# Kernel tuning notes

Hardware: AMD Instinct MI355X
Metric: run time of the kernel (lower is better)

Reference implementation:

```python
import jax, jax.numpy as jnp
import numpy as np

DIM = 1024
HEADS = 16
HEAD_DIM = DIM // HEADS
THRESH = 0.29514
SHARP = 15.0
LN_EPS = 1e-5
NORM_EPS = 1e-12


def setup_inputs() -> dict:
    key = jax.random.key(0)
    ks = jax.random.split(key, 8)
    s = 1.0 / np.sqrt(DIM)
    sg = 1.0 / np.sqrt(HEAD_DIM)
    return {
        "x": jax.random.normal(ks[0], (2, 2048, DIM), dtype=jnp.float32),
        "Wq": jax.random.uniform(ks[1], (DIM, DIM), jnp.float32, -s, s),
        "Wk": jax.random.uniform(ks[2], (DIM, DIM), jnp.float32, -s, s),
        "Wv": jax.random.uniform(ks[3], (DIM, DIM), jnp.float32, -s, s),
        "gq": jax.random.uniform(ks[4], (HEAD_DIM,), jnp.float32, -sg, sg),
        "gk": jax.random.uniform(ks[5], (HEAD_DIM,), jnp.float32, -sg, sg),
        "Wo": jax.random.uniform(ks[6], (DIM, DIM), jnp.float32, -s, s),
        "bo": jax.random.uniform(ks[7], (DIM,), jnp.float32, -s, s),
        "ln_w": jnp.ones((DIM,), jnp.float32),
        "ln_b": jnp.zeros((DIM,), jnp.float32),
    }


def _l2norm(t):
    # F.normalize: t / max(||t||_2, eps)
    n = jnp.sqrt(jnp.sum(t * t, axis=-1, keepdims=True))
    return t / jnp.maximum(n, NORM_EPS)


def reference(x, Wq, Wk, Wv, gq, gk, Wo, bo, ln_w, ln_b):
    B, T, D = x.shape
    # LayerNorm over last dim
    mu = jnp.mean(x, axis=-1, keepdims=True)
    var = jnp.mean((x - mu) ** 2, axis=-1, keepdims=True)
    x_norm = (x - mu) / jnp.sqrt(var + LN_EPS) * ln_w + ln_b

    def split_heads(t):  # [B,T,D] -> [B,H,T,hd]
        return t.reshape(B, T, HEADS, HEAD_DIM).transpose(0, 2, 1, 3)

    q = _l2norm(split_heads(x_norm @ Wq))
    k = _l2norm(split_heads(x_norm @ Wk))
    v = split_heads(x @ Wv)  # note: v uses un-normalized x, as in source

    align = jnp.einsum("bhtd,bhsd->bhts", q, k)  # cosine alignment
    resonance = jax.nn.sigmoid((align - THRESH) * SHARP)
    gate_q = jnp.einsum("bhtd,d->bht", q, gq)
    gate_k = jnp.einsum("bhsd,d->bhs", k, gk)
    modulation = resonance * gate_q[..., :, None] * gate_k[..., None, :]
    collapse = jnp.einsum("bhts,bhsd->bhtd", modulation, v)
    collapse = collapse.transpose(0, 2, 1, 3).reshape(B, T, D)
    return collapse @ Wo + bo
```

## Files before the change

### kernel.cpp

```cpp
#include <hip/hip_runtime.h>
#include <math.h>

#define DIM 1024
#define T_SEQ 2048
#define NBATCH 2
#define HEADS 16
#define HD 64
#define NTOK 4096
#define THRESH 0.29514f
#define SHARP 15.0f
#define LOG2E 1.4426950408889634f

typedef __attribute__((ext_vector_type(8))) short bf16x8;
typedef __attribute__((ext_vector_type(4))) float f32x4;
typedef __attribute__((ext_vector_type(4))) unsigned int u32x4;

__device__ __forceinline__ unsigned short f2b(float f) {
    unsigned int u = __float_as_uint(f);
    unsigned int r = (u + 0x7FFFu + ((u >> 16) & 1u)) >> 16;
    return (unsigned short)r;
}
__device__ __forceinline__ float b2f(unsigned short u) {
    return __uint_as_float(((unsigned int)u) << 16);
}
__device__ __forceinline__ unsigned int pack2_bf16(float lo, float hi) {
    unsigned int a = __float_as_uint(lo) + 0x8000u;
    unsigned int b = __float_as_uint(hi) + 0x8000u;
    return __builtin_amdgcn_perm(b, a, 0x07060302u);
}

__device__ __forceinline__ void async_cp16(const unsigned short* g, unsigned short* l) {
    __builtin_amdgcn_global_load_lds(
        (const __attribute__((address_space(1))) unsigned int*)g,
        (__attribute__((address_space(3))) unsigned int*)l, 16, 0, 0);
}

__global__ __launch_bounds__(256) void ln_xnorm_kernel(
    const float* __restrict__ x, const float* __restrict__ lnw, const float* __restrict__ lnb,
    unsigned short* __restrict__ xnb, unsigned short* __restrict__ xb) {
    int row = blockIdx.x * 4 + (threadIdx.x >> 6);
    int lane = threadIdx.x & 63;
    const float4* xr = (const float4*)(x + (size_t)row * DIM);
    float4 v[4];
    float s = 0.f, ss = 0.f;
#pragma unroll
    for (int i = 0; i < 4; i++) {
        v[i] = xr[lane + i * 64];
        s += v[i].x + v[i].y + v[i].z + v[i].w;
        ss += v[i].x * v[i].x + v[i].y * v[i].y + v[i].z * v[i].z + v[i].w * v[i].w;
    }
#pragma unroll
    for (int off = 32; off; off >>= 1) {
        s += __shfl_xor(s, off);
        ss += __shfl_xor(ss, off);
    }
    float m = s * (1.f / DIM);
    float rstd = rsqrtf(ss * (1.f / DIM) - m * m + 1e-5f);
#pragma unroll
    for (int i = 0; i < 4; i++) {
        int e = (lane + i * 64) * 4;
        float4 lw = *(const float4*)&lnw[e];
        float4 lb = *(const float4*)&lnb[e];
        ushort4 un, ur;
        un.x = f2b((v[i].x - m) * rstd * lw.x + lb.x);
        un.y = f2b((v[i].y - m) * rstd * lw.y + lb.y);
        un.z = f2b((v[i].z - m) * rstd * lw.z + lb.z);
        un.w = f2b((v[i].w - m) * rstd * lw.w + lb.w);
        ur.x = f2b(v[i].x); ur.y = f2b(v[i].y); ur.z = f2b(v[i].z); ur.w = f2b(v[i].w);
        *(ushort4*)&xnb[(size_t)row * DIM + e] = un;
        *(ushort4*)&xb[(size_t)row * DIM + e] = ur;
    }
}

__global__ __launch_bounds__(256) void wtrans_kernel(
    const float* __restrict__ W0, const float* __restrict__ W1,
    const float* __restrict__ W2, const float* __restrict__ W3,
    unsigned short* __restrict__ T0, unsigned short* __restrict__ T1,
    unsigned short* __restrict__ T2, unsigned short* __restrict__ T3) {
    __shared__ float tile[64][65];
    const int z = blockIdx.z;
    const float* W = (z == 0) ? W0 : (z == 1) ? W1 : (z == 2) ? W2 : W3;
    unsigned short* T = (z == 0) ? T0 : (z == 1) ? T1 : (z == 2) ? T2 : T3;
    const int k0 = blockIdx.x * 64, n0 = blockIdx.y * 64;
    const int r = threadIdx.x >> 3;
    const int c = (threadIdx.x & 7) * 8;
#pragma unroll
    for (int half = 0; half < 2; half++) {
        int rr = r + half * 32;
        float4 a = *(const float4*)&W[(size_t)(k0 + rr) * DIM + n0 + c];
        float4 b = *(const float4*)&W[(size_t)(k0 + rr) * DIM + n0 + c + 4];
        tile[rr][c + 0] = a.x; tile[rr][c + 1] = a.y; tile[rr][c + 2] = a.z; tile[rr][c + 3] = a.w;
        tile[rr][c + 4] = b.x; tile[rr][c + 5] = b.y; tile[rr][c + 6] = b.z; tile[rr][c + 7] = b.w;
    }
    __syncthreads();
#pragma unroll
    for (int half = 0; half < 2; half++) {
        int dd = r + half * 32;
        bf16x8 o;
#pragma unroll
        for (int j = 0; j < 8; j++) o[j] = (short)f2b(tile[c + j][dd]);
        *(bf16x8*)&T[(size_t)(n0 + dd) * DIM + k0 + c] = o;
    }
}

template <int MODE>
__global__ __launch_bounds__(256) void gemm_mfma_kernel(
    const unsigned short* __restrict__ A0, const unsigned short* __restrict__ A2,
    const unsigned short* __restrict__ Bt0, const unsigned short* __restrict__ Bt1,
    const unsigned short* __restrict__ Bt2, const float* __restrict__ bias,
    const float* __restrict__ gq, const float* __restrict__ gk,
    unsigned short* __restrict__ Oq, unsigned short* __restrict__ Ok,
    unsigned short* __restrict__ Ov, float* __restrict__ gq_t, float* __restrict__ gk_t,
    float* __restrict__ Oout) {
    constexpr int NT = (MODE == 0) ? 4 : 2;
    __shared__ __align__(16) unsigned short As[2][128 * 32];
    __shared__ __align__(16) unsigned short Bs[2][NT * 32 * 32];
    const int tid = threadIdx.x;
    const int lane = tid & 63, w = tid >> 6;
    const int l16 = lane & 15, quad = lane >> 4;
    const int wm = w >> 1, wn = w & 1;
    int m0, n0, z = 0;
    if constexpr (MODE == 0) {
        const int f = blockIdx.x + (blockIdx.y << 5) + (blockIdx.z << 8);
        const int ww = (f & 7) * 96 + (f >> 3);
        z = ww >> 8;
        m0 = ((ww >> 3) & 31) * 128;
        n0 = (ww & 7) * 128;
    } else {
        const int f = blockIdx.x + (blockIdx.y << 5);
        const int ww = (f & 7) * 64 + (f >> 3);
        m0 = (ww >> 4) * 128;
        n0 = (ww & 15) * 64;
    }
    const unsigned short* A;
    const unsigned short* Bt;
    if constexpr (MODE == 0) {
        A = (z == 2) ? A2 : A0;
        Bt = (z == 0) ? Bt0 : (z == 1) ? Bt1 : Bt2;
    } else {
        A = A0;
        Bt = Bt0;
    }
    f32x4 acc[4][NT] = {};
    const int kswz = (l16 >> 1) & 3;

    const int lin0 = tid, lin1 = 256 + tid;
    const int sm0 = lin0 >> 2, sk0 = (lin0 & 3) ^ ((sm0 >> 1) & 3);
    const int sm1 = lin1 >> 2, sk1 = (lin1 & 3) ^ ((sm1 >> 1) & 3);

    auto stage = [&](int kb, int k0) {
        async_cp16(A + (size_t)(m0 + sm0) * DIM + k0 + sk0 * 8, &As[kb][lin0 * 8]);
        async_cp16(A + (size_t)(m0 + sm1) * DIM + k0 + sk1 * 8, &As[kb][lin1 * 8]);
        async_cp16(Bt + (size_t)(n0 + sm0) * DIM + k0 + sk0 * 8, &Bs[kb][lin0 * 8]);
        if constexpr (MODE == 0)
            async_cp16(Bt + (size_t)(n0 + sm1) * DIM + k0 + sk1 * 8, &Bs[kb][lin1 * 8]);
    };

    stage(0, 0);
    __syncthreads();

    for (int ks = 0; ks < DIM / 32; ks++) {
        const int cur = ks & 1;
        if (ks + 1 < DIM / 32) stage(cur ^ 1, (ks + 1) * 32);
        bf16x8 af[4], bfr[NT];
#pragma unroll
        for (int t = 0; t < 4; t++) {
            int ma = wm * 64 + t * 16 + l16;
            af[t] = *(const bf16x8*)(&As[cur][ma * 32 + ((quad ^ kswz) * 8)]);
        }
#pragma unroll
        for (int t = 0; t < NT; t++) {
            int nb = wn * (NT * 16) + t * 16 + l16;
            bfr[t] = *(const bf16x8*)(&Bs[cur][nb * 32 + ((quad ^ kswz) * 8)]);
        }
#pragma unroll
        for (int mt = 0; mt < 4; mt++)
#pragma unroll
            for (int nt = 0; nt < NT; nt++)
                acc[mt][nt] =
                    __builtin_amdgcn_mfma_f32_16x16x32_bf16(af[mt], bfr[nt], acc[mt][nt], 0, 0, 0);
        __syncthreads();
    }

    if constexpr (MODE == 0) {
        const int h = (n0 + wn * 64) >> 6;
        if (z <= 1) {
            constexpr float QSCALE = -SHARP * LOG2E;
            const float* gvec = (z == 0) ? gq : gk;
            float* gate = (z == 0) ? gq_t : gk_t;
            unsigned short* O = (z == 0) ? Oq : Ok;
            const float oscale = (z == 0) ? QSCALE : 1.0f;
            float gv[4];
#pragma unroll
            for (int nt = 0; nt < 4; nt++) gv[nt] = gvec[nt * 16 + l16];
#pragma unroll
            for (int mt = 0; mt < 4; mt++) {
#pragma unroll
                for (int r = 0; r < 4; r++) {
                    float ss = 0.f;
#pragma unroll
                    for (int nt = 0; nt < 4; nt++) ss += acc[mt][nt][r] * acc[mt][nt][r];
#pragma unroll
                    for (int msk = 1; msk < 16; msk <<= 1) ss += __shfl_xor(ss, msk);
                    float rn = __builtin_amdgcn_rcpf(fmaxf(sqrtf(ss), 1e-12f));
                    float vn[4], gg = 0.f;
#pragma unroll
                    for (int nt = 0; nt < 4; nt++) {
                        vn[nt] = acc[mt][nt][r] * rn;
                        gg += vn[nt] * gv[nt];
                    }
#pragma unroll
                    for (int msk = 1; msk < 16; msk <<= 1) gg += __shfl_xor(gg, msk);
                    int tok = m0 + wm * 64 + mt * 16 + quad * 4 + r;
                    int b = tok >> 11, t = tok & 2047;
                    size_t rowbase = ((size_t)(b * HEADS + h) * T_SEQ + t) * HD;
#pragma unroll
                    for (int nt = 0; nt < 4; nt++)
                        O[rowbase + nt * 16 + l16] = f2b(vn[nt] * oscale);
                    if (l16 == 0) gate[(b * HEADS + h) * T_SEQ + t] = gg;
                }
            }
        } else {
#pragma unroll
            for (int mt = 0; mt < 4; mt++) {
#pragma unroll
                for (int r = 0; r < 4; r++) {
                    int tok = m0 + wm * 64 + mt * 16 + quad * 4 + r;
                    int b = tok >> 11, t = tok & 2047;
                    size_t rowbase = ((size_t)(b * HEADS + h) * T_SEQ + t) * HD;
#pragma unroll
                    for (int nt = 0; nt < 4; nt++)
                        Ov[rowbase + nt * 16 + l16] = f2b(acc[mt][nt][r]);
                }
            }
        }
    } else {
        float bias_r[NT];
#pragma unroll
        for (int nt = 0; nt < NT; nt++) bias_r[nt] = bias[n0 + wn * (NT * 16) + nt * 16 + l16];
#pragma unroll
        for (int mt = 0; mt < 4; mt++) {
#pragma unroll
            for (int r = 0; r < 4; r++) {
                int tok = m0 + wm * 64 + mt * 16 + quad * 4 + r;
#pragma unroll
                for (int nt = 0; nt < NT; nt++) {
                    int n = n0 + wn * (NT * 16) + nt * 16 + l16;
                    Oout[(size_t)tok * DIM + n] = acc[mt][nt][r] + bias_r[nt];
                }
            }
        }
    }
}

__global__ __launch_bounds__(256) void vtrans_kernel(const unsigned short* __restrict__ Vn,
                                                     const float* __restrict__ gk_t,
                                                     unsigned short* __restrict__ Vt) {
    __shared__ float tile[64][65];
    const int bh = blockIdx.y;
    const int t0 = blockIdx.x * 64;
    const int r = threadIdx.x >> 3;
    const int c = (threadIdx.x & 7) * 8;
    const unsigned short* src = Vn + (size_t)bh * T_SEQ * HD;
#pragma unroll
    for (int half = 0; half < 2; half++) {
        int rr = r + half * 32;
        float gkv = gk_t[bh * T_SEQ + t0 + rr];
        bf16x8 v = *(const bf16x8*)(src + (size_t)(t0 + rr) * HD + c);
#pragma unroll
        for (int j = 0; j < 8; j++) tile[rr][c + j] = b2f((unsigned short)v[j]) * gkv;
    }
    __syncthreads();
    unsigned short* dst = Vt + (size_t)bh * HD * T_SEQ;
#pragma unroll
    for (int half = 0; half < 2; half++) {
        int dd = r + half * 32;
        bf16x8 o;
#pragma unroll
        for (int j = 0; j < 8; j++) o[j] = (short)f2b(tile[c + j][dd]);
        *(bf16x8*)(dst + (size_t)dd * T_SEQ + t0 + c) = o;
    }
}

__global__ __launch_bounds__(256, 4) void attn_mfma_kernel(
    const unsigned short* __restrict__ Qn, const unsigned short* __restrict__ Kn,
    const unsigned short* __restrict__ Vt, const float* __restrict__ gateq,
    unsigned short* __restrict__ collp0, unsigned short* __restrict__ collp1) {
    __shared__ __align__(16) unsigned short Ks[2][64 * 64];
    __shared__ __align__(16) unsigned short VtL[2][64 * 64];
    const int tid = threadIdx.x;
    const int lane = tid & 63, w = tid >> 6;
    const int quad = lane >> 4, l16 = lane & 15;
    const int f = blockIdx.x + 16 * blockIdx.y + 256 * blockIdx.z;
    const int q_ = f >> 3;
    const int panel = (f & 7) * 8 + (q_ >> 4);
    const int t0 = (q_ & 15) * 128;
    const int h = panel & 15;
    const int zz = panel >> 4;
    const int b = zz >> 1, shalf = zz & 1;
    const int sbase = shalf * (T_SEQ / 2);
    const int bh = b * HEADS + h;
    const size_t base = (size_t)bh * T_SEQ * HD;
    constexpr float K0 = THRESH * SHARP * LOG2E;
    const f32x4 k0v = {K0, K0, K0, K0};

    int det0 = quad, det1 = quad + 4;
    asm("v_permlane16_swap_b32 %0, %1" : "+v"(det0), "+v"(det1));
    const bool flagA = (__builtin_amdgcn_readfirstlane(det0) == 0);

    bf16x8 fq[2][2];
#pragma unroll
    for (int mt = 0; mt < 2; mt++) {
        const unsigned short* qrow = Qn + base + (size_t)(t0 + w * 32 + mt * 16 + l16) * HD;
        fq[mt][0] = *(const bf16x8*)(qrow + quad * 8);
        fq[mt][1] = *(const bf16x8*)(qrow + 32 + quad * 8);
    }

    f32x4 oacc[4][2] = {};
    const int srow = tid >> 3;
    const int sgp = tid & 7;
    const int swz = l16 & 7;

    auto stage_chunk = [&](unsigned short* ksn, unsigned short* vtn, int s0) {
#pragma unroll
        for (int half = 0; half < 2; half++) {
            int row = srow + half * 32;
            int g = sgp ^ (row & 7);
            async_cp16(Kn + base + (size_t)(s0 + row) * HD + g * 8, ksn + row * 64 + sgp * 8);
            async_cp16(Vt + base + (size_t)row * T_SEQ + s0 + g * 8, vtn + row * 64 + sgp * 8);
        }
    };

    auto do_chunk = [&](const unsigned short* ksb, const unsigned short* vtb) {
#pragma unroll
        for (int kh = 0; kh < 2; kh++) {
            unsigned int p[2][2][2];
#pragma unroll
            for (int ct2 = 0; ct2 < 2; ct2++) {
                const int ct = 2 * kh + ct2;
                const unsigned short* krow = ksb + (ct * 16 + l16) * 64;
                bf16x8 fk0 = *(const bf16x8*)(krow + (quad ^ swz) * 8);
                bf16x8 fk1 = *(const bf16x8*)(krow + ((quad + 4) ^ swz) * 8);
#pragma unroll
                for (int mt = 0; mt < 2; mt++) {
                    __builtin_amdgcn_s_setprio(1);
                    f32x4 s1 =
                        __builtin_amdgcn_mfma_f32_16x16x32_bf16(fk0, fq[mt][0], k0v, 0, 0, 0);
                    f32x4 sacc =
                        __builtin_amdgcn_mfma_f32_16x16x32_bf16(fk1, fq[mt][1], s1, 0, 0, 0);
                    __builtin_amdgcn_s_setprio(0);
                    float w0 = __builtin_amdgcn_rcpf(1.f + __builtin_amdgcn_exp2f(sacc[0]));
                    float w1 = __builtin_amdgcn_rcpf(1.f + __builtin_amdgcn_exp2f(sacc[1]));
                    float w2 = __builtin_amdgcn_rcpf(1.f + __builtin_amdgcn_exp2f(sacc[2]));
                    float w3 = __builtin_amdgcn_rcpf(1.f + __builtin_amdgcn_exp2f(sacc[3]));
                    p[mt][ct2][0] = pack2_bf16(w0, w1);
                    p[mt][ct2][1] = pack2_bf16(w2, w3);
                }
            }
            int gv = (4 * kh + 2 * (quad & 1) + (quad >> 1)) ^ swz;
            bf16x8 fv[4];
#pragma unroll
            for (int dt = 0; dt < 4; dt++)
                fv[dt] = *(const bf16x8*)(vtb + (dt * 16 + l16) * 64 + gv * 8);
#pragma unroll
            for (int mt = 0; mt < 2; mt++) {
                unsigned int aL = p[mt][0][0], aH = p[mt][0][1];
                unsigned int bL = p[mt][1][0], bH = p[mt][1][1];
                asm("v_permlane16_swap_b32 %0, %1" : "+v"(aL), "+v"(bL));
                asm("v_permlane16_swap_b32 %0, %1" : "+v"(aH), "+v"(bH));
                u32x4 bt;
                if (flagA) {
                    bt.x = aL; bt.y = aH; bt.z = bL; bt.w = bH;
                } else {
                    bt.x = bL; bt.y = bH; bt.z = aL; bt.w = aH;
                }
                bf16x8 fs = __builtin_bit_cast(bf16x8, bt);
                __builtin_amdgcn_s_setprio(1);
#pragma unroll
                for (int dt = 0; dt < 4; dt++)
                    oacc[dt][mt] =
                        __builtin_amdgcn_mfma_f32_16x16x32_bf16(fv[dt], fs, oacc[dt][mt], 0, 0, 0);
                __builtin_amdgcn_s_setprio(0);
            }
        }
        __syncthreads();
    };

    stage_chunk(&Ks[0][0], &VtL[0][0], sbase);
    __syncthreads();

    for (int j = 0; j < T_SEQ / 256; j++) {
        stage_chunk(&Ks[1][0], &VtL[1][0], sbase + j * 128 + 64);
        do_chunk(&Ks[0][0], &VtL[0][0]);
        if (j + 1 < T_SEQ / 256) stage_chunk(&Ks[0][0], &VtL[0][0], sbase + j * 128 + 128);
        do_chunk(&Ks[1][0], &VtL[1][0]);
    }

    unsigned short* collp = shalf ? collp1 : collp0;
#pragma unroll
    for (int mt = 0; mt < 2; mt++) {
        int t = t0 + w * 32 + mt * 16 + l16;
        float gq_v = gateq[bh * T_SEQ + t];
        unsigned short* dst = collp + ((size_t)b * T_SEQ + t) * DIM + h * HD;
#pragma unroll
        for (int dt = 0; dt < 4; dt++) {
            ushort4 o;
            o.x = f2b(oacc[dt][mt][0] * gq_v);
            o.y = f2b(oacc[dt][mt][1] * gq_v);
            o.z = f2b(oacc[dt][mt][2] * gq_v);
            o.w = f2b(oacc[dt][mt][3] * gq_v);
            *(ushort4*)(dst + dt * 16 + quad * 4) = o;
        }
    }
}

__global__ __launch_bounds__(256) void merge_kernel(unsigned short* __restrict__ p0,
                                                    const unsigned short* __restrict__ p1) {
    size_t i = ((size_t)blockIdx.x * 256 + threadIdx.x) * 8;
    bf16x8 a = *(const bf16x8*)(p0 + i);
    bf16x8 c = *(const bf16x8*)(p1 + i);
    bf16x8 o;
#pragma unroll
    for (int j = 0; j < 8; j++)
        o[j] = (short)f2b(b2f((unsigned short)a[j]) + b2f((unsigned short)c[j]));
    *(bf16x8*)(p0 + i) = o;
}

extern "C" void kernel_launch(void* const* d_in, const int* in_sizes, int n_in,
                              void* d_out, int out_size, void* d_ws, size_t ws_size,
                              hipStream_t stream) {
    const float* x = (const float*)d_in[0];
    const float* Wq = (const float*)d_in[1];
    const float* Wk = (const float*)d_in[2];
    const float* Wv = (const float*)d_in[3];
    const float* gq = (const float*)d_in[4];
    const float* gk = (const float*)d_in[5];
    const float* Wo = (const float*)d_in[6];
    const float* bo = (const float*)d_in[7];
    const float* lnw = (const float*)d_in[8];
    const float* lnb = (const float*)d_in[9];
    float* out = (float*)d_out;

    unsigned short* ws = (unsigned short*)d_ws;
    unsigned short* xnb = ws;
    unsigned short* xb = xnb + (size_t)NTOK * DIM;
    unsigned short* Wqt = xb + (size_t)NTOK * DIM;
    unsigned short* Wkt = Wqt + (size_t)DIM * DIM;
    unsigned short* Wvt = Wkt + (size_t)DIM * DIM;
    unsigned short* Wot = Wvt + (size_t)DIM * DIM;
    unsigned short* Q16 = Wot + (size_t)DIM * DIM;
    unsigned short* K16 = Q16 + (size_t)NTOK * DIM;
    unsigned short* Vn = K16 + (size_t)NTOK * DIM;
    float* gq_t = (float*)(Vn + (size_t)NTOK * DIM);
    float* gk_t = gq_t + NBATCH * HEADS * T_SEQ;
    unsigned short* collb1 = (unsigned short*)(gk_t + NBATCH * HEADS * T_SEQ);
    unsigned short* Vt = xnb;
    unsigned short* collb0 = xb;

    ln_xnorm_kernel<<<NTOK / 4, 256, 0, stream>>>(x, lnw, lnb, xnb, xb);
    wtrans_kernel<<<dim3(16, 16, 4), 256, 0, stream>>>(Wq, Wk, Wv, Wo, Wqt, Wkt, Wvt, Wot);
    gemm_mfma_kernel<0><<<dim3(NTOK / 128, DIM / 128, 3), 256, 0, stream>>>(
        xnb, xb, Wqt, Wkt, Wvt, nullptr, gq, gk, Q16, K16, Vn, gq_t, gk_t, nullptr);
    vtrans_kernel<<<dim3(T_SEQ / 64, NBATCH * HEADS), 256, 0, stream>>>(Vn, gk_t, Vt);
    attn_mfma_kernel<<<dim3(T_SEQ / 128, HEADS, NBATCH * 2), 256, 0, stream>>>(
        Q16, K16, Vt, gq_t, collb0, collb1);
    merge_kernel<<<(NTOK * DIM) / (256 * 8), 256, 0, stream>>>(collb0, collb1);
    gemm_mfma_kernel<1><<<dim3(NTOK / 128, DIM / 64, 1), 256, 0, stream>>>(
        collb0, nullptr, Wot, nullptr, nullptr, bo, nullptr, nullptr, nullptr, nullptr, nullptr,
        nullptr, nullptr, out);
}
```

Before: 222.0 us.

## Fuse LN and weight-transpose launches; fold split-K merge into output GEMM A-load

Merges the LayerNorm and weight-transpose kernels into a single launch that branches on block index. It also removes the separate merge kernel by having the output-projection GEMM read both partial attention outputs through registers, sum them, and write the result to LDS. This replaces its async copy for A. The aim is to save two launches and one full read-write pass over the collapse buffer. The cost is that the output GEMM's A loads become synchronous register loads with extra conversion ALU, and each row is re-summed once per N tile.

```diff
diff --git a/kernel.cpp b/kernel.cpp
--- a/kernel.cpp
+++ b/kernel.cpp
@@ -35,71 +35,72 @@
         (__attribute__((address_space(3))) unsigned int*)l, 16, 0, 0);
 }
 
-__global__ __launch_bounds__(256) void ln_xnorm_kernel(
+__global__ __launch_bounds__(256) void prep_kernel(
     const float* __restrict__ x, const float* __restrict__ lnw, const float* __restrict__ lnb,
-    unsigned short* __restrict__ xnb, unsigned short* __restrict__ xb) {
-    int row = blockIdx.x * 4 + (threadIdx.x >> 6);
-    int lane = threadIdx.x & 63;
-    const float4* xr = (const float4*)(x + (size_t)row * DIM);
-    float4 v[4];
-    float s = 0.f, ss = 0.f;
-#pragma unroll
-    for (int i = 0; i < 4; i++) {
-        v[i] = xr[lane + i * 64];
-        s += v[i].x + v[i].y + v[i].z + v[i].w;
-        ss += v[i].x * v[i].x + v[i].y * v[i].y + v[i].z * v[i].z + v[i].w * v[i].w;
-    }
-#pragma unroll
-    for (int off = 32; off; off >>= 1) {
-        s += __shfl_xor(s, off);
-        ss += __shfl_xor(ss, off);
-    }
-    float m = s * (1.f / DIM);
-    float rstd = rsqrtf(ss * (1.f / DIM) - m * m + 1e-5f);
-#pragma unroll
-    for (int i = 0; i < 4; i++) {
-        int e = (lane + i * 64) * 4;
-        float4 lw = *(const float4*)&lnw[e];
-        float4 lb = *(const float4*)&lnb[e];
-        ushort4 un, ur;
-        un.x = f2b((v[i].x - m) * rstd * lw.x + lb.x);
-        un.y = f2b((v[i].y - m) * rstd * lw.y + lb.y);
-        un.z = f2b((v[i].z - m) * rstd * lw.z + lb.z);
-        un.w = f2b((v[i].w - m) * rstd * lw.w + lb.w);
-        ur.x = f2b(v[i].x); ur.y = f2b(v[i].y); ur.z = f2b(v[i].z); ur.w = f2b(v[i].w);
-        *(ushort4*)&xnb[(size_t)row * DIM + e] = un;
-        *(ushort4*)&xb[(size_t)row * DIM + e] = ur;
-    }
-}
-
-__global__ __launch_bounds__(256) void wtrans_kernel(
+    unsigned short* __restrict__ xnb, unsigned short* __restrict__ xb,
     const float* __restrict__ W0, const float* __restrict__ W1,
     const float* __restrict__ W2, const float* __restrict__ W3,
     unsigned short* __restrict__ T0, unsigned short* __restrict__ T1,
     unsigned short* __restrict__ T2, unsigned short* __restrict__ T3) {
     __shared__ float tile[64][65];
-    const int z = blockIdx.z;
-    const float* W = (z == 0) ? W0 : (z == 1) ? W1 : (z == 2) ? W2 : W3;
-    unsigned short* T = (z == 0) ? T0 : (z == 1) ? T1 : (z == 2) ? T2 : T3;
-    const int k0 = blockIdx.x * 64, n0 = blockIdx.y * 64;
-    const int r = threadIdx.x >> 3;
-    const int c = (threadIdx.x & 7) * 8;
-#pragma unroll
-    for (int half = 0; half < 2; half++) {
-        int rr = r + half * 32;
-        float4 a = *(const float4*)&W[(size_t)(k0 + rr) * DIM + n0 + c];
-        float4 b = *(const float4*)&W[(size_t)(k0 + rr) * DIM + n0 + c + 4];
-        tile[rr][c + 0] = a.x; tile[rr][c + 1] = a.y; tile[rr][c + 2] = a.z; tile[rr][c + 3] = a.w;
-        tile[rr][c + 4] = b.x; tile[rr][c + 5] = b.y; tile[rr][c + 6] = b.z; tile[rr][c + 7] = b.w;
-    }
-    __syncthreads();
-#pragma unroll
-    for (int half = 0; half < 2; half++) {
-        int dd = r + half * 32;
-        bf16x8 o;
-#pragma unroll
-        for (int j = 0; j < 8; j++) o[j] = (short)f2b(tile[c + j][dd]);
-        *(bf16x8*)&T[(size_t)(n0 + dd) * DIM + k0 + c] = o;
+    if (blockIdx.x < 1024) {
+        int row = blockIdx.x * 4 + (threadIdx.x >> 6);
+        int lane = threadIdx.x & 63;
+        const float4* xr = (const float4*)(x + (size_t)row * DIM);
+        float4 v[4];
+        float s = 0.f, ss = 0.f;
+#pragma unroll
+        for (int i = 0; i < 4; i++) {
+            v[i] = xr[lane + i * 64];
+            s += v[i].x + v[i].y + v[i].z + v[i].w;
+            ss += v[i].x * v[i].x + v[i].y * v[i].y + v[i].z * v[i].z + v[i].w * v[i].w;
+        }
+#pragma unroll
+        for (int off = 32; off; off >>= 1) {
+            s += __shfl_xor(s, off);
+            ss += __shfl_xor(ss, off);
+        }
+        float m = s * (1.f / DIM);
+        float rstd = rsqrtf(ss * (1.f / DIM) - m * m + 1e-5f);
+#pragma unroll
+        for (int i = 0; i < 4; i++) {
+            int e = (lane + i * 64) * 4;
+            float4 lw = *(const float4*)&lnw[e];
+            float4 lb = *(const float4*)&lnb[e];
+            ushort4 un, ur;
+            un.x = f2b((v[i].x - m) * rstd * lw.x + lb.x);
+            un.y = f2b((v[i].y - m) * rstd * lw.y + lb.y);
+            un.z = f2b((v[i].z - m) * rstd * lw.z + lb.z);
+            un.w = f2b((v[i].w - m) * rstd * lw.w + lb.w);
+            ur.x = f2b(v[i].x); ur.y = f2b(v[i].y); ur.z = f2b(v[i].z); ur.w = f2b(v[i].w);
+            *(ushort4*)&xnb[(size_t)row * DIM + e] = un;
+            *(ushort4*)&xb[(size_t)row * DIM + e] = ur;
+        }
+    } else {
+        const int i = blockIdx.x - 1024;
+        const int z = i >> 8;
+        const int k0 = ((i >> 4) & 15) * 64, n0 = (i & 15) * 64;
+        const float* W = (z == 0) ? W0 : (z == 1) ? W1 : (z == 2) ? W2 : W3;
+        unsigned short* T = (z == 0) ? T0 : (z == 1) ? T1 : (z == 2) ? T2 : T3;
+        const int r = threadIdx.x >> 3;
+        const int c = (threadIdx.x & 7) * 8;
+#pragma unroll
+        for (int half = 0; half < 2; half++) {
+            int rr = r + half * 32;
+            float4 a = *(const float4*)&W[(size_t)(k0 + rr) * DIM + n0 + c];
+            float4 b = *(const float4*)&W[(size_t)(k0 + rr) * DIM + n0 + c + 4];
+            tile[rr][c + 0] = a.x; tile[rr][c + 1] = a.y; tile[rr][c + 2] = a.z; tile[rr][c + 3] = a.w;
+            tile[rr][c + 4] = b.x; tile[rr][c + 5] = b.y; tile[rr][c + 6] = b.z; tile[rr][c + 7] = b.w;
+        }
+        __syncthreads();
+#pragma unroll
+        for (int half = 0; half < 2; half++) {
+            int dd = r + half * 32;
+            bf16x8 o;
+#pragma unroll
+            for (int j = 0; j < 8; j++) o[j] = (short)f2b(tile[c + j][dd]);
+            *(bf16x8*)&T[(size_t)(n0 + dd) * DIM + k0 + c] = o;
+        }
     }
 }
 
@@ -148,20 +149,48 @@
     const int sm0 = lin0 >> 2, sk0 = (lin0 & 3) ^ ((sm0 >> 1) & 3);
     const int sm1 = lin1 >> 2, sk1 = (lin1 & 3) ^ ((sm1 >> 1) & 3);
 
-    auto stage = [&](int kb, int k0) {
-        async_cp16(A + (size_t)(m0 + sm0) * DIM + k0 + sk0 * 8, &As[kb][lin0 * 8]);
-        async_cp16(A + (size_t)(m0 + sm1) * DIM + k0 + sk1 * 8, &As[kb][lin1 * 8]);
+    auto stage_async = [&](int kb, int k0) {
         async_cp16(Bt + (size_t)(n0 + sm0) * DIM + k0 + sk0 * 8, &Bs[kb][lin0 * 8]);
-        if constexpr (MODE == 0)
+        if constexpr (MODE == 0) {
             async_cp16(Bt + (size_t)(n0 + sm1) * DIM + k0 + sk1 * 8, &Bs[kb][lin1 * 8]);
+            async_cp16(A + (size_t)(m0 + sm0) * DIM + k0 + sk0 * 8, &As[kb][lin0 * 8]);
+            async_cp16(A + (size_t)(m0 + sm1) * DIM + k0 + sk1 * 8, &As[kb][lin1 * 8]);
+        }
     };
 
-    stage(0, 0);
+    bf16x8 pa0, pa1, pc0, pc1;
+    auto loadA = [&](int k0) {
+        const size_t o0 = (size_t)(m0 + sm0) * DIM + k0 + sk0 * 8;
+        const size_t o1 = (size_t)(m0 + sm1) * DIM + k0 + sk1 * 8;
+        pa0 = *(const bf16x8*)(A + o0);
+        pc0 = *(const bf16x8*)(A2 + o0);
+        pa1 = *(const bf16x8*)(A + o1);
+        pc1 = *(const bf16x8*)(A2 + o1);
+    };
+    auto writeA = [&](int kb) {
+        bf16x8 o0, o1;
+#pragma unroll
+        for (int j = 0; j < 8; j++) {
+            o0[j] = (short)f2b(b2f((unsigned short)pa0[j]) + b2f((unsigned short)pc0[j]));
+            o1[j] = (short)f2b(b2f((unsigned short)pa1[j]) + b2f((unsigned short)pc1[j]));
+        }
+        *(bf16x8*)(&As[kb][lin0 * 8]) = o0;
+        *(bf16x8*)(&As[kb][lin1 * 8]) = o1;
+    };
+
+    stage_async(0, 0);
+    if constexpr (MODE == 1) {
+        loadA(0);
+        writeA(0);
+    }
     __syncthreads();
 
     for (int ks = 0; ks < DIM / 32; ks++) {
         const int cur = ks & 1;
-        if (ks + 1 < DIM / 32) stage(cur ^ 1, (ks + 1) * 32);
+        if (ks + 1 < DIM / 32) {
+            stage_async(cur ^ 1, (ks + 1) * 32);
+            if constexpr (MODE == 1) loadA((ks + 1) * 32);
+        }
         bf16x8 af[4], bfr[NT];
 #pragma unroll
         for (int t = 0; t < 4; t++) {
@@ -179,6 +208,9 @@
             for (int nt = 0; nt < NT; nt++)
                 acc[mt][nt] =
                     __builtin_amdgcn_mfma_f32_16x16x32_bf16(af[mt], bfr[nt], acc[mt][nt], 0, 0, 0);
+        if constexpr (MODE == 1) {
+            if (ks + 1 < DIM / 32) writeA(cur ^ 1);
+        }
         __syncthreads();
     }
 
@@ -414,18 +446,6 @@
     }
 }
 
-__global__ __launch_bounds__(256) void merge_kernel(unsigned short* __restrict__ p0,
-                                                    const unsigned short* __restrict__ p1) {
-    size_t i = ((size_t)blockIdx.x * 256 + threadIdx.x) * 8;
-    bf16x8 a = *(const bf16x8*)(p0 + i);
-    bf16x8 c = *(const bf16x8*)(p1 + i);
-    bf16x8 o;
-#pragma unroll
-    for (int j = 0; j < 8; j++)
-        o[j] = (short)f2b(b2f((unsigned short)a[j]) + b2f((unsigned short)c[j]));
-    *(bf16x8*)(p0 + i) = o;
-}
-
 extern "C" void kernel_launch(void* const* d_in, const int* in_sizes, int n_in,
                               void* d_out, int out_size, void* d_ws, size_t ws_size,
                               hipStream_t stream) {
@@ -457,15 +477,14 @@
     unsigned short* Vt = xnb;
     unsigned short* collb0 = xb;
 
-    ln_xnorm_kernel<<<NTOK / 4, 256, 0, stream>>>(x, lnw, lnb, xnb, xb);
-    wtrans_kernel<<<dim3(16, 16, 4), 256, 0, stream>>>(Wq, Wk, Wv, Wo, Wqt, Wkt, Wvt, Wot);
+    prep_kernel<<<2048, 256, 0, stream>>>(x, lnw, lnb, xnb, xb, Wq, Wk, Wv, Wo, Wqt, Wkt, Wvt,
+                                          Wot);
     gemm_mfma_kernel<0><<<dim3(NTOK / 128, DIM / 128, 3), 256, 0, stream>>>(
         xnb, xb, Wqt, Wkt, Wvt, nullptr, gq, gk, Q16, K16, Vn, gq_t, gk_t, nullptr);
     vtrans_kernel<<<dim3(T_SEQ / 64, NBATCH * HEADS), 256, 0, stream>>>(Vn, gk_t, Vt);
     attn_mfma_kernel<<<dim3(T_SEQ / 128, HEADS, NBATCH * 2), 256, 0, stream>>>(
         Q16, K16, Vt, gq_t, collb0, collb1);
-    merge_kernel<<<(NTOK * DIM) / (256 * 8), 256, 0, stream>>>(collb0, collb1);
     gemm_mfma_kernel<1><<<dim3(NTOK / 128, DIM / 64, 1), 256, 0, stream>>>(
-        collb0, nullptr, Wot, nullptr, nullptr, bo, nullptr, nullptr, nullptr, nullptr, nullptr,
+        collb0, collb1, Wot, nullptr, nullptr, bo, nullptr, nullptr, nullptr, nullptr, nullptr,
         nullptr, nullptr, out);
 }
```

Result: no change. 225.1 us (+1.4%).
